# Performance work log

Measured on AMD Instinct MI355X. Metric: run time of the kernel, lower is better.

The kernel has to match this reference:

```python
import jax, jax.numpy as jnp
import numpy as np
from jax import lax

PERIODS = [1, 2, 4, 8]
N = 128  # output_dim // len(periods)
INPUT_DIM = 512
OUTPUT_DIM = 512
BATCH = 64
SEQ = 512


def setup_inputs() -> dict:
    key = jax.random.key(0)
    ks = jax.random.split(key, 32)
    inp = {}
    inp['x'] = jax.random.normal(ks[0], (BATCH, SEQ, INPUT_DIM), dtype=jnp.float32)
    s = 0.05
    inp['W'] = jax.random.normal(ks[1], (INPUT_DIM, OUTPUT_DIM), dtype=jnp.float32) * s
    inp['b'] = jnp.zeros((OUTPUT_DIM,), dtype=jnp.float32)
    inp['Wr'] = jax.random.normal(ks[2], (INPUT_DIM, OUTPUT_DIM), dtype=jnp.float32) * s
    inp['br'] = jnp.zeros((OUTPUT_DIM,), dtype=jnp.float32)
    inp['Wz'] = jax.random.normal(ks[3], (INPUT_DIM, OUTPUT_DIM), dtype=jnp.float32) * s
    inp['bz'] = jnp.zeros((OUTPUT_DIM,), dtype=jnp.float32)
    kidx = 4
    for i in range(len(PERIODS)):
        m = (i + 1) * N
        inp[f'clock_h_{i}'] = jax.random.normal(ks[kidx], (m, N), dtype=jnp.float32) * (1.0 / np.sqrt(m)); kidx += 1
        inp[f'clock_r_{i}'] = jax.random.normal(ks[kidx], (m, m), dtype=jnp.float32) * (1.0 / np.sqrt(m)); kidx += 1
        inp[f'clock_z_{i}'] = jax.random.normal(ks[kidx], (m, N), dtype=jnp.float32) * (1.0 / np.sqrt(m)); kidx += 1
    return inp


def _forward(x, W, b, Wr, br, Wz, bz, clock_h, clock_r, clock_z):
    # x: [B, S, D_in] -> time-major [S, B, D_in]
    Xt = jnp.transpose(x, (1, 0, 2))
    xt = Xt @ W + b      # [S, B, D]
    xrt = Xt @ Wr + br   # [S, B, D]
    xzt = Xt @ Wz + bz   # [S, B, D]
    B = x.shape[0]
    D = W.shape[1]

    def step(h, inputs):
        t, x_t, x_rt, x_zt = inputs
        blocks = []
        for i, period in enumerate(PERIODS):
            m = (i + 1) * N
            hp = h[:, :m]                 # [B, (i+1)n]
            nah = h[:, i * N:(i + 1) * N] # [B, n]
            r = jax.nn.sigmoid(x_rt[:, :m] + hp @ clock_r[i])
            z = jax.nn.sigmoid(x_zt[:, i * N:(i + 1) * N] + hp @ clock_z[i])
            h_new = jax.nn.sigmoid(x_t[:, i * N:(i + 1) * N] + (r * hp) @ clock_h[i])
            v = z * h_new + (1.0 - z) * nah
            blocks.append(jnp.where(t % period == 0, v, nah))
        h_t = jnp.concatenate(blocks, axis=1)
        return h_t, h_t

    times = jnp.arange(x.shape[1])
    h0 = jnp.zeros((B, D), dtype=x.dtype)
    _, hs = lax.scan(step, h0, (times, xt, xrt, xzt))
    # return_sequences=True: back to batch-major [B, S, D]
    return jnp.transpose(hs, (1, 0, 2))


def reference(x, W, b, Wr, br, Wz, bz,
              clock_h_0, clock_r_0, clock_z_0,
              clock_h_1, clock_r_1, clock_z_1,
              clock_h_2, clock_r_2, clock_z_2,
              clock_h_3, clock_r_3, clock_z_3):
    clock_h = [clock_h_0, clock_h_1, clock_h_2, clock_h_3]
    clock_r = [clock_r_0, clock_r_1, clock_r_2, clock_r_3]
    clock_z = [clock_z_0, clock_z_1, clock_z_2, clock_z_3]
    return _forward(x, W, b, Wr, br, Wz, bz, clock_h, clock_r, clock_z)
```

## Files before the change

### kernel.cpp

```cpp
#include <hip/hip_runtime.h>

#define SEQ   512
#define BATCH 64
#define DIM   512

typedef float  f32x4 __attribute__((ext_vector_type(4)));
typedef short  s16x8 __attribute__((ext_vector_type(8)));
typedef __bf16 bf16x2 __attribute__((ext_vector_type(2)));

__device__ __forceinline__ float bits2f(unsigned u) {
  union { unsigned u; float f; } v; v.u = u; return v.f;
}
__device__ __forceinline__ float bf2f(unsigned short h) { return bits2f((unsigned)h << 16); }
__device__ __forceinline__ float bflo(unsigned u) { return bits2f(u << 16); }
__device__ __forceinline__ float bfhi(unsigned u) { return bits2f(u & 0xFFFF0000u); }
__device__ __forceinline__ unsigned short f2bf(float f) {
  union { float f; unsigned u; } v; v.f = f;
  unsigned r = v.u + 0x7FFFu + ((v.u >> 16) & 1u);
  return (unsigned short)(r >> 16);
}
__device__ __forceinline__ unsigned packbf(float lo, float hi) {
  return (unsigned)f2bf(lo) | ((unsigned)f2bf(hi) << 16);
}
__device__ __forceinline__ float sigm(float x) { return 1.0f / (1.0f + __expf(-x)); }

__device__ __forceinline__ float dot2(unsigned w, unsigned h, float acc) {
#if __has_builtin(__builtin_amdgcn_fdot2_f32_bf16)
  return __builtin_amdgcn_fdot2_f32_bf16(__builtin_bit_cast(bf16x2, w),
                                         __builtin_bit_cast(bf16x2, h), acc, false);
#else
  return acc + bflo(w) * bflo(h) + bfhi(w) * bfhi(h);
#endif
}

__device__ __forceinline__ void bar_lds() {
  asm volatile("s_waitcnt lgkmcnt(0)" ::: "memory");
  __builtin_amdgcn_s_barrier();
  asm volatile("" ::: "memory");
}

#define NJOBS 18
struct CastJobs {
  const float* src[NJOBS];
  const float* src2[NJOBS];
  void*        dst[NJOBS];
  int          n[NJOBS];
  int          mode[NJOBS];
  int          m[NJOBS];
  int          iN[NJOBS];
};

__global__ __launch_bounds__(256) void cast_kernel(CastJobs jobs) {
  int gsz = gridDim.x * blockDim.x;
  int gid = blockIdx.x * blockDim.x + threadIdx.x;
  for (int j = 0; j < NJOBS; ++j) {
    int n = jobs.n[j], mode = jobs.mode[j];
    int m = jobs.m[j], iN = jobs.iN[j];
    const float* s = jobs.src[j];
    if (mode == 1) {
      unsigned short* d = (unsigned short*)jobs.dst[j];
      for (int i = gid; i < n; i += gsz) {
        int k = i >> 9, nn = i & 511;
        d[nn * 512 + k] = f2bf(s[i]);
      }
    } else if (mode == 3) {
      unsigned* d = (unsigned*)jobs.dst[j];
      for (int i = gid; i < n; i += gsz) {
        int k2 = i / m, jj = i - k2 * m;
        d[i] = packbf(s[(iN + 2 * k2) * m + jj], s[(iN + 2 * k2 + 1) * m + jj]);
      }
    } else if (mode == 4) {
      unsigned* d = (unsigned*)jobs.dst[j];
      for (int i = gid; i < n; i += gsz) {
        int k2 = i >> 7, jj = i & 127;
        d[i] = packbf(s[(2 * k2) * 128 + jj], s[(2 * k2 + 1) * 128 + jj]);
      }
    } else if (mode == 5) {
      unsigned* d = (unsigned*)jobs.dst[j];
      for (int i = gid; i < n; i += gsz) {
        int k2 = i >> 7, jj = i & 127;
        d[i] = packbf(s[(iN + 2 * k2) * 128 + jj], s[(iN + 2 * k2 + 1) * 128 + jj]);
      }
    } else if (mode == 6) {
      const float* s2 = jobs.src2[j];
      unsigned short* d = (unsigned short*)jobs.dst[j];
      for (int i = gid; i < n; i += gsz) {
        int nrow = i / iN, k = i - nrow * iN;
        float v = (nrow < m) ? s[k * m + nrow] : s2[k * 128 + (nrow - m)];
        d[i] = f2bf(v);
      }
    }
  }
}

__global__ __launch_bounds__(256) void proj_kernel(
    const float* __restrict__ x,
    const unsigned short* __restrict__ WbT,
    const float* __restrict__ bias0, const float* __restrict__ bias1,
    const float* __restrict__ bias2,
    unsigned short* __restrict__ p0, unsigned short* __restrict__ p1,
    unsigned short* __restrict__ p2)
{
  __shared__ __align__(16) unsigned short aS[64 * 40];
  __shared__ __align__(16) unsigned short bS[128 * 40];

  int bx = blockIdx.x;
  int nt = bx % 12, t = bx / 12;
  int wsel = nt >> 2, ncol0 = (nt & 3) * 128;
  const float* bias = (wsel == 0) ? bias0 : (wsel == 1 ? bias1 : bias2);
  unsigned short* pout = (wsel == 0) ? p0 : (wsel == 1 ? p1 : p2);

  int tid = threadIdx.x;
  int wv = tid >> 6, lane = tid & 63;
  int lq = lane & 15, quad = lane >> 4;

  f32x4 acc[8];
#pragma unroll
  for (int s = 0; s < 8; ++s) acc[s] = (f32x4){0.f, 0.f, 0.f, 0.f};

  int arow = tid >> 2, ak0 = (tid & 3) * 8;
  const float* asrc0 = x + ((size_t)arow * SEQ + t) * DIM + ak0;
  int brow = tid >> 1, bk0 = (tid & 1) * 16;
  const unsigned short* bsrc0 =
      WbT + ((size_t)(wsel * 512 + ncol0 + brow)) * 512 + bk0;

  for (int kk = 0; kk < 16; ++kk) {
    const float* asrc = asrc0 + kk * 32;
    float4 f0 = *(const float4*)(asrc);
    float4 f1 = *(const float4*)(asrc + 4);
    uint4 av;
    av.x = packbf(f0.x, f0.y);
    av.y = packbf(f0.z, f0.w);
    av.z = packbf(f1.x, f1.y);
    av.w = packbf(f1.z, f1.w);
    *(uint4*)(aS + arow * 40 + ak0) = av;
    const unsigned short* bsrc = bsrc0 + kk * 32;
    *(uint4*)(bS + brow * 40 + bk0)     = *(const uint4*)(bsrc);
    *(uint4*)(bS + brow * 40 + bk0 + 8) = *(const uint4*)(bsrc + 8);
    __syncthreads();

    s16x8 af = *(const s16x8*)(aS + (wv * 16 + lq) * 40 + quad * 8);
#pragma unroll
    for (int s = 0; s < 8; ++s) {
      s16x8 bf = *(const s16x8*)(bS + (s * 16 + lq) * 40 + quad * 8);
      acc[s] = __builtin_amdgcn_mfma_f32_16x16x32_bf16(af, bf, acc[s], 0, 0, 0);
    }
    __syncthreads();
  }

#pragma unroll
  for (int s = 0; s < 8; ++s) {
    int col = ncol0 + s * 16 + lq;
    float bv = bias[col];
#pragma unroll
    for (int v = 0; v < 4; ++v) {
      int b = wv * 16 + quad * 4 + v;
      pout[((size_t)(t * BATCH + b)) * DIM + col] = f2bf(acc[s][v] + bv);
    }
  }
}

template<int I>
__global__ __launch_bounds__(256) void base_gemm(
    const float* __restrict__ outp,
    const unsigned short* __restrict__ Bcat,
    unsigned short* __restrict__ baseO)
{
  constexpr int KI  = 4 * I;
  constexpr int K   = 128 * I;
  constexpr int NT  = I + 2;
  constexpr int NW  = NT * 128;
  constexpr int PER = 1 << I;

  __shared__ __align__(16) unsigned short aS[64 * 40];
  __shared__ __align__(16) unsigned short bS[128 * 40];

  int bx = blockIdx.x;
  int nt = bx % NT, n = bx / NT;
  int ncol0 = nt * 128;

  int tid = threadIdx.x;
  int wv = tid >> 6, lane = tid & 63;
  int lq = lane & 15, quad = lane >> 4;

  f32x4 acc[8];
#pragma unroll
  for (int s = 0; s < 8; ++s) acc[s] = (f32x4){0.f, 0.f, 0.f, 0.f};

  int arow = tid >> 2, ak0 = (tid & 3) * 8;
  const float* asrc0 = outp + ((size_t)arow * SEQ + (n * PER - 1)) * DIM + ak0;
  int brow = tid >> 1, bk0 = (tid & 1) * 16;
  const unsigned short* bsrc0 = Bcat + (size_t)(ncol0 + brow) * K + bk0;

  for (int kk = 0; kk < KI; ++kk) {
    uint4 av;
    if (n > 0) {
      const float* asrc = asrc0 + kk * 32;
      float4 f0 = *(const float4*)(asrc);
      float4 f1 = *(const float4*)(asrc + 4);
      av.x = packbf(f0.x, f0.y);
      av.y = packbf(f0.z, f0.w);
      av.z = packbf(f1.x, f1.y);
      av.w = packbf(f1.z, f1.w);
    } else {
      av = (uint4){0u, 0u, 0u, 0u};
    }
    *(uint4*)(aS + arow * 40 + ak0) = av;
    const unsigned short* bsrc = bsrc0 + kk * 32;
    *(uint4*)(bS + brow * 40 + bk0)     = *(const uint4*)(bsrc);
    *(uint4*)(bS + brow * 40 + bk0 + 8) = *(const uint4*)(bsrc + 8);
    __syncthreads();

    s16x8 af = *(const s16x8*)(aS + (wv * 16 + lq) * 40 + quad * 8);
#pragma unroll
    for (int s = 0; s < 8; ++s) {
      s16x8 bf = *(const s16x8*)(bS + (s * 16 + lq) * 40 + quad * 8);
      acc[s] = __builtin_amdgcn_mfma_f32_16x16x32_bf16(af, bf, acc[s], 0, 0, 0);
    }
    __syncthreads();
  }

#pragma unroll
  for (int s = 0; s < 8; ++s) {
    int col = ncol0 + s * 16 + lq;
#pragma unroll
    for (int v = 0; v < 4; ++v) {
      int bb = wv * 16 + quad * 4 + v;
      baseO[(size_t)(n * 64 + bb) * NW + col] = f2bf(acc[s][v]);
    }
  }
}

template<int I, int TPB>
__global__ __launch_bounds__(TPB, 1) void scan_phase(
    const unsigned short* __restrict__ px,
    const unsigned short* __restrict__ pr,
    const unsigned short* __restrict__ pz,
    const unsigned* __restrict__ crpk,
    const unsigned* __restrict__ czpk,
    const unsigned* __restrict__ chpk,
    const unsigned short* __restrict__ base,
    float* __restrict__ out)
{
  constexpr int M   = (I + 1) * 128;
  constexpr int IN  = I * 128;
  constexpr int PER = 1 << I;
  constexpr int U   = 512 >> I;
  constexpr int NW  = M + 128;
  constexpr int HKP = M / 2;
  constexpr int SPL = (I == 0) ? 2 : 4;
  constexpr int HT  = HKP / SPL;
  constexpr int ZT  = 64 / SPL;
  constexpr int RTH = (M < TPB) ? M : TPB;

  __shared__ __align__(16) float    hS[128];
  __shared__ __align__(16) unsigned hPk[64];
  __shared__ __align__(16) unsigned uPk[HKP];

  const int b  = blockIdx.x;
  const int t  = threadIdx.x;
  const int jh = t / SPL;
  const int q  = t % SPL;
  const bool hasR = (t < RTH);
  const int col0 = t;

  unsigned wr0[64];
  if (hasR) {
#pragma unroll
    for (int k2 = 0; k2 < 64; ++k2) wr0[k2] = crpk[k2 * M + col0];
  }
  unsigned wz[ZT];
#pragma unroll
  for (int k2 = 0; k2 < ZT; ++k2) wz[k2] = czpk[(q * ZT + k2) * 128 + jh];
  unsigned wh[HT];
#pragma unroll
  for (int k2 = 0; k2 < HT; ++k2) wh[k2] = chpk[(q * HT + k2) * 128 + jh];

  if (t < 128) hS[t] = 0.f;
  if (t < 64)  hPk[t] = 0u;
  float vprev = 0.f;

  unsigned short f_pr = 0, f_pz = 0, f_px = 0, f_br = 0, f_bz = 0;
  float f_pv = 0.f;
  {
    f_pz = (pz + (size_t)b * DIM)[IN + jh];
    f_px = (px + (size_t)b * DIM)[IN + jh];
    if (hasR) f_pr = (pr + (size_t)b * DIM)[col0];
    if constexpr (I > 0) {
      const unsigned short* baseR = base + (size_t)b * NW;
      if (hasR) f_br = baseR[col0];
      f_bz = baseR[M + jh];
    }
  }

  bar_lds();

  for (int n = 0; n < U; ++n) {
    const int s = n * PER;
    const unsigned short c_pr = f_pr, c_pz = f_pz, c_px = f_px;
    const unsigned short c_br = f_br, c_bz = f_bz;
    const float c_pv = f_pv;

    {
      const int n2 = (n + 1 < U) ? (n + 1) : n;
      const int s2 = n2 * PER;
      f_pz = (pz + ((size_t)(s2 * BATCH + b)) * DIM)[IN + jh];
      f_px = (px + ((size_t)(s2 * BATCH + b)) * DIM)[IN + jh];
      if (hasR) f_pr = (pr + ((size_t)(s2 * BATCH + b)) * DIM)[col0];
      if constexpr (I > 0) {
        const unsigned short* baseR = base + (size_t)(n2 * 64 + b) * NW;
        if (hasR) f_br = baseR[col0];
        f_bz = baseR[M + jh];
        if (hasR && col0 < IN)
          f_pv = (out + ((size_t)b * SEQ + (s2 - 1)) * DIM)[col0];
      }
    }

    float az0 = 0.f, az1 = 0.f;
#pragma unroll
    for (int k2 = 0; k2 < ZT; k2 += 2) {
      az0 = dot2(wz[k2],     hPk[q * ZT + k2],     az0);
      az1 = dot2(wz[k2 + 1], hPk[q * ZT + k2 + 1], az1);
    }
    float az = az0 + az1;
    az += __shfl_xor(az, 1);
    if constexpr (SPL == 4) az += __shfl_xor(az, 2);
    float zpre = bf2f(c_pz) + az;
    if constexpr (I > 0) zpre += bf2f(c_bz);
    const float zg = sigm(zpre);

    float u = 0.f;
    if (hasR) {
      float a0 = 0.f, a1 = 0.f, a2 = 0.f, a3 = 0.f;
#pragma unroll
      for (int k2 = 0; k2 < 64; k2 += 4) {
        a0 = dot2(wr0[k2],     hPk[k2],     a0);
        a1 = dot2(wr0[k2 + 1], hPk[k2 + 1], a1);
        a2 = dot2(wr0[k2 + 2], hPk[k2 + 2], a2);
        a3 = dot2(wr0[k2 + 3], hPk[k2 + 3], a3);
      }
      float ar = bf2f(c_pr) + (a0 + a1) + (a2 + a3);
      if constexpr (I > 0) ar += bf2f(c_br);
      const float r = sigm(ar);
      float hp;
      if constexpr (I == 0) hp = hS[col0];
      else hp = (col0 >= IN) ? hS[col0 - IN] : c_pv;
      u = r * hp;
    }
    const float uo = __shfl_xor(u, 1);
    if (hasR && !(t & 1)) uPk[t >> 1] = packbf(u, uo);

    bar_lds();

    float ah0 = 0.f, ah1 = 0.f, ah2 = 0.f, ah3 = 0.f;
    {
      const int o = q * HT;
#pragma unroll
      for (int k2 = 0; k2 < HT; k2 += 4) {
        ah0 = dot2(wh[k2],     uPk[o + k2],     ah0);
        ah1 = dot2(wh[k2 + 1], uPk[o + k2 + 1], ah1);
        ah2 = dot2(wh[k2 + 2], uPk[o + k2 + 2], ah2);
        ah3 = dot2(wh[k2 + 3], uPk[o + k2 + 3], ah3);
      }
    }
    float ah = (ah0 + ah1) + (ah2 + ah3);
    ah += __shfl_xor(ah, 1);
    if constexpr (SPL == 4) ah += __shfl_xor(ah, 2);
    const float hnew = sigm(ah + bf2f(c_px));
    const float v = zg * hnew + (1.f - zg) * vprev;
    vprev = v;

    if (q == 0) hS[jh] = v;
    const float vp = __shfl_xor(v, SPL);
    if ((t & (2 * SPL - 1)) == 0) hPk[t / (2 * SPL)] = packbf(v, vp);

    float* orow = out + ((size_t)b * SEQ + s) * DIM + IN + jh;
#pragma unroll
    for (int p = q; p < PER; p += SPL) orow[p * DIM] = v;

    bar_lds();
  }
}

extern "C" void kernel_launch(void* const* d_in, const int* in_sizes, int n_in,
                              void* d_out, int out_size, void* d_ws, size_t ws_size,
                              hipStream_t stream) {
  (void)in_sizes; (void)n_in; (void)out_size; (void)ws_size;

  const float* x  = (const float*)d_in[0];
  const float* W  = (const float*)d_in[1];
  const float* bb = (const float*)d_in[2];
  const float* Wr = (const float*)d_in[3];
  const float* br = (const float*)d_in[4];
  const float* Wz = (const float*)d_in[5];
  const float* bz = (const float*)d_in[6];
  const float* ch_[4]; const float* cr_[4]; const float* cz_[4];
  for (int i = 0; i < 4; ++i) {
    ch_[i] = (const float*)d_in[7 + 3 * i];
    cr_[i] = (const float*)d_in[8 + 3 * i];
    cz_[i] = (const float*)d_in[9 + 3 * i];
  }

  char* ws = (char*)d_ws;
  size_t off = 0;
  auto alloc = [&](size_t bytes) -> void* {
    void* p = ws + off;
    off += (bytes + 255) & ~(size_t)255;
    return p;
  };

  unsigned short* WbT = (unsigned short*)alloc(3ull * 512 * 512 * 2);
  unsigned* Crpk[4]; unsigned* Chpk[4]; unsigned* Czpk[4];
  unsigned short* Bcat[4] = {nullptr, nullptr, nullptr, nullptr};
  for (int i = 0; i < 4; ++i) {
    int m = (i + 1) * 128;
    Crpk[i] = (unsigned*)alloc((size_t)64 * m * 4);
    Chpk[i] = (unsigned*)alloc((size_t)(m / 2) * 128 * 4);
    Czpk[i] = (unsigned*)alloc((size_t)64 * 128 * 4);
  }
  for (int i = 1; i < 4; ++i) {
    int m = (i + 1) * 128, iN = i * 128;
    Bcat[i] = (unsigned short*)alloc((size_t)(m + 128) * iN * 2);
  }
  unsigned short* p0 = (unsigned short*)alloc((size_t)SEQ * BATCH * DIM * 2);
  unsigned short* p1 = (unsigned short*)alloc((size_t)SEQ * BATCH * DIM * 2);
  unsigned short* p2 = (unsigned short*)alloc((size_t)SEQ * BATCH * DIM * 2);
  unsigned short* baseB = (unsigned short*)alloc((size_t)16384 * 384 * 2);

  CastJobs jobs{};
  int jn = 0;
  const float* wsrc[3] = {W, Wr, Wz};
  for (int j = 0; j < 3; ++j) {
    jobs.src[jn] = wsrc[j]; jobs.dst[jn] = WbT + (size_t)j * 512 * 512;
    jobs.n[jn] = 512 * 512; jobs.mode[jn] = 1; jobs.m[jn] = 512; jobs.iN[jn] = 0; jn++;
  }
  for (int i = 0; i < 4; ++i) {
    int m = (i + 1) * 128, iN = i * 128;
    jobs.src[jn] = cr_[i]; jobs.dst[jn] = Crpk[i];
    jobs.n[jn] = 64 * m; jobs.mode[jn] = 3; jobs.m[jn] = m; jobs.iN[jn] = iN; jn++;
    jobs.src[jn] = ch_[i]; jobs.dst[jn] = Chpk[i];
    jobs.n[jn] = (m / 2) * 128; jobs.mode[jn] = 4; jobs.m[jn] = m; jobs.iN[jn] = iN; jn++;
    jobs.src[jn] = cz_[i]; jobs.dst[jn] = Czpk[i];
    jobs.n[jn] = 64 * 128; jobs.mode[jn] = 5; jobs.m[jn] = m; jobs.iN[jn] = iN; jn++;
  }
  for (int i = 1; i < 4; ++i) {
    int m = (i + 1) * 128, iN = i * 128;
    jobs.src[jn] = cr_[i]; jobs.src2[jn] = cz_[i]; jobs.dst[jn] = Bcat[i];
    jobs.n[jn] = (m + 128) * iN; jobs.mode[jn] = 6; jobs.m[jn] = m; jobs.iN[jn] = iN; jn++;
  }
  cast_kernel<<<256, 256, 0, stream>>>(jobs);

  proj_kernel<<<SEQ * 12, 256, 0, stream>>>(x, WbT, bb, br, bz, p0, p1, p2);

  float* outp = (float*)d_out;

  scan_phase<0, 256><<<64, 256, 0, stream>>>(p0, p1, p2, Crpk[0], Czpk[0],
                                             Chpk[0], nullptr, outp);
  base_gemm<1><<<256 * 3, 256, 0, stream>>>(outp, Bcat[1], baseB);
  scan_phase<1, 512><<<64, 512, 0, stream>>>(p0, p1, p2, Crpk[1], Czpk[1],
                                             Chpk[1], baseB, outp);
  base_gemm<2><<<128 * 4, 256, 0, stream>>>(outp, Bcat[2], baseB);
  scan_phase<2, 512><<<64, 512, 0, stream>>>(p0, p1, p2, Crpk[2], Czpk[2],
                                             Chpk[2], baseB, outp);
  base_gemm<3><<<64 * 5, 256, 0, stream>>>(outp, Bcat[3], baseB);
  scan_phase<3, 512><<<64, 512, 0, stream>>>(p0, p1, p2, Crpk[3], Czpk[3],
                                             Chpk[3], baseB, outp);
}
```

Measured before the change: 1.514 ms.

## Replace phase-0 scan with LDS-resident weights and warp-specialized r/z/h roles

```diff
diff --git a/kernel.cpp b/kernel.cpp
--- a/kernel.cpp
+++ b/kernel.cpp
@@ -33,13 +33,17 @@
 #endif
 }
 
+__device__ __forceinline__ unsigned bcast(unsigned v, int k2) {
+  return (unsigned)__builtin_amdgcn_readlane((int)v, k2);
+}
+
 __device__ __forceinline__ void bar_lds() {
   asm volatile("s_waitcnt lgkmcnt(0)" ::: "memory");
   __builtin_amdgcn_s_barrier();
   asm volatile("" ::: "memory");
 }
 
-#define NJOBS 18
+#define NJOBS 21
 struct CastJobs {
   const float* src[NJOBS];
   const float* src2[NJOBS];
@@ -88,6 +92,12 @@
         int nrow = i / iN, k = i - nrow * iN;
         float v = (nrow < m) ? s[k * m + nrow] : s2[k * 128 + (nrow - m)];
         d[i] = f2bf(v);
+      }
+    } else if (mode == 7) {
+      unsigned* d = (unsigned*)jobs.dst[j];
+      for (int i = gid; i < n; i += gsz) {
+        int c = i >> 6, k2 = i & 63;
+        d[i] = packbf(s[(2 * k2) * 128 + c], s[(2 * k2 + 1) * 128 + c]);
       }
     }
   }
@@ -228,6 +238,117 @@
       int bb = wv * 16 + quad * 4 + v;
       baseO[(size_t)(n * 64 + bb) * NW + col] = f2bf(acc[s][v]);
     }
+  }
+}
+
+#define SCAN0_LDS_BYTES 67072
+
+__global__ __launch_bounds__(384, 1) void scan0_lds(
+    const unsigned short* __restrict__ px,
+    const unsigned short* __restrict__ pr,
+    const unsigned short* __restrict__ pz,
+    const unsigned* __restrict__ CrT,
+    const unsigned* __restrict__ CzT,
+    const unsigned* __restrict__ ChT,
+    float* __restrict__ out)
+{
+  extern __shared__ __align__(16) unsigned char dynLDS[];
+  unsigned* wLDS = (unsigned*)dynLDS;
+  float*    hF   = (float*)(dynLDS + 65536);
+  unsigned* hX   = (unsigned*)(dynLDS + 66048);
+  unsigned* uX   = (unsigned*)(dynLDS + 66304);
+  float*    zX   = (float*)(dynLDS + 66560);
+
+  const int b    = blockIdx.x;
+  const int t    = threadIdx.x;
+  const int lane = t & 63;
+  const bool isR = (t < 128);
+  const bool isH = (t >= 256);
+  const int  jz  = t - 128;
+  const int  jj  = t - 256;
+
+  for (int idx = t; idx < 2 * 128 * 16; idx += 384) {
+    int a = idx >> 11;
+    int rem = idx & 2047;
+    int c = rem >> 4, kq = rem & 15;
+    const unsigned* src = (a == 0) ? CrT : ChT;
+    uint4 v = *(const uint4*)(src + c * 64 + kq * 4);
+    *(uint4*)(wLDS + a * 8192 + c * 64 + (((kq ^ (c & 7)) << 2))) = v;
+  }
+  if (t < 128) hF[t] = 0.f;
+  if (t < 64)  hX[t] = 0u;
+
+  unsigned short f_p;
+  const unsigned short* pp;
+  if (isR)       { f_p = pr[(size_t)b * DIM + t];  pp = pr + ((size_t)BATCH + b) * DIM + t;  }
+  else if (!isH) { f_p = pz[(size_t)b * DIM + jz]; pp = pz + ((size_t)BATCH + b) * DIM + jz; }
+  else           { f_p = px[(size_t)b * DIM + jj]; pp = px + ((size_t)BATCH + b) * DIM + jj; }
+
+  float vprev = 0.f;
+
+  bar_lds();
+
+#pragma unroll 1
+  for (int s = 0; s < SEQ; ++s) {
+    const unsigned short c_p = f_p;
+    if (s + 1 < SEQ) { f_p = *pp; pp += (size_t)BATCH * DIM; }
+
+    if (!isH) {
+      const unsigned hpk = hX[lane];
+      float a0 = 0.f, a1 = 0.f, a2 = 0.f, a3 = 0.f;
+      if (isR) {
+        const unsigned* wb = wLDS + t * 64;
+        const int sw = (t & 7) << 2;
+#pragma unroll
+        for (int kq = 0; kq < 16; ++kq) {
+          uint4 wv = *(const uint4*)(wb + ((kq << 2) ^ sw));
+          a0 = dot2(wv.x, bcast(hpk, 4 * kq + 0), a0);
+          a1 = dot2(wv.y, bcast(hpk, 4 * kq + 1), a1);
+          a2 = dot2(wv.z, bcast(hpk, 4 * kq + 2), a2);
+          a3 = dot2(wv.w, bcast(hpk, 4 * kq + 3), a3);
+        }
+        const float r = sigm(bf2f(c_p) + (a0 + a1) + (a2 + a3));
+        const float u = r * hF[t];
+        const float uo = __shfl_xor(u, 1);
+        if (!(t & 1)) uX[t >> 1] = packbf(u, uo);
+      } else {
+        const uint4* czp = (const uint4*)(CzT + jz * 64);
+#pragma unroll
+        for (int kq = 0; kq < 16; ++kq) {
+          uint4 wv = czp[kq];
+          a0 = dot2(wv.x, bcast(hpk, 4 * kq + 0), a0);
+          a1 = dot2(wv.y, bcast(hpk, 4 * kq + 1), a1);
+          a2 = dot2(wv.z, bcast(hpk, 4 * kq + 2), a2);
+          a3 = dot2(wv.w, bcast(hpk, 4 * kq + 3), a3);
+        }
+        zX[jz] = sigm(bf2f(c_p) + (a0 + a1) + (a2 + a3));
+      }
+    }
+    bar_lds();
+
+    if (isH) {
+      const unsigned upk = uX[lane];
+      const float zf = zX[jj];
+      const unsigned* wb = wLDS + 8192 + jj * 64;
+      const int sw = (jj & 7) << 2;
+      float a0 = 0.f, a1 = 0.f, a2 = 0.f, a3 = 0.f;
+#pragma unroll
+      for (int kq = 0; kq < 16; ++kq) {
+        uint4 wv = *(const uint4*)(wb + ((kq << 2) ^ sw));
+        a0 = dot2(wv.x, bcast(upk, 4 * kq + 0), a0);
+        a1 = dot2(wv.y, bcast(upk, 4 * kq + 1), a1);
+        a2 = dot2(wv.z, bcast(upk, 4 * kq + 2), a2);
+        a3 = dot2(wv.w, bcast(upk, 4 * kq + 3), a3);
+      }
+      const float hnew = sigm(bf2f(c_p) + (a0 + a1) + (a2 + a3));
+      const float v = zf * hnew + (1.f - zf) * vprev;
+      vprev = v;
+      hF[jj] = v;
+      const float vo = __shfl_xor(v, 1);
+      if (!(jj & 1)) hX[jj >> 1] = packbf(v, vo);
+      out[((size_t)b * SEQ + s) * DIM + jj] = v;
+    }
+    bar_lds();
   }
 }
 
@@ -253,9 +374,9 @@
   constexpr int ZT  = 64 / SPL;
   constexpr int RTH = (M < TPB) ? M : TPB;
 
-  __shared__ __align__(16) float    hS[128];
-  __shared__ __align__(16) unsigned hPk[64];
-  __shared__ __align__(16) unsigned uPk[HKP];
+  __shared__ float    hS[128];
+  __shared__ unsigned hPk[64];
+  __shared__ unsigned uPk[HKP];
 
   const int b  = blockIdx.x;
   const int t  = threadIdx.x;
@@ -344,7 +465,7 @@
       const float r = sigm(ar);
       float hp;
       if constexpr (I == 0) hp = hS[col0];
-      else hp = (col0 >= IN) ? hS[col0 - IN] : c_pv;
+      else hp = (col0 >= IN) ? hS[col0 - IN] : (n > 0 ? c_pv : 0.f);
       u = r * hp;
     }
     const float uo = __shfl_xor(u, 1);
@@ -422,6 +543,9 @@
     int m = (i + 1) * 128, iN = i * 128;
     Bcat[i] = (unsigned short*)alloc((size_t)(m + 128) * iN * 2);
   }
+  unsigned* CrT0 = (unsigned*)alloc((size_t)128 * 64 * 4);
+  unsigned* CzT0 = (unsigned*)alloc((size_t)128 * 64 * 4);
+  unsigned* ChT0 = (unsigned*)alloc((size_t)128 * 64 * 4);
   unsigned short* p0 = (unsigned short*)alloc((size_t)SEQ * BATCH * DIM * 2);
   unsigned short* p1 = (unsigned short*)alloc((size_t)SEQ * BATCH * DIM * 2);
   unsigned short* p2 = (unsigned short*)alloc((size_t)SEQ * BATCH * DIM * 2);
@@ -448,14 +572,32 @@
     jobs.src[jn] = cr_[i]; jobs.src2[jn] = cz_[i]; jobs.dst[jn] = Bcat[i];
     jobs.n[jn] = (m + 128) * iN; jobs.mode[jn] = 6; jobs.m[jn] = m; jobs.iN[jn] = iN; jn++;
   }
+  jobs.src[jn] = cr_[0]; jobs.dst[jn] = CrT0;
+  jobs.n[jn] = 128 * 64; jobs.mode[jn] = 7; jobs.m[jn] = 128; jobs.iN[jn] = 0; jn++;
+  jobs.src[jn] = cz_[0]; jobs.dst[jn] = CzT0;
+  jobs.n[jn] = 128 * 64; jobs.mode[jn] = 7; jobs.m[jn] = 128; jobs.iN[jn] = 0; jn++;
+  jobs.src[jn] = ch_[0]; jobs.dst[jn] = ChT0;
+  jobs.n[jn] = 128 * 64; jobs.mode[jn] = 7; jobs.m[jn] = 128; jobs.iN[jn] = 0; jn++;
   cast_kernel<<<256, 256, 0, stream>>>(jobs);
 
   proj_kernel<<<SEQ * 12, 256, 0, stream>>>(x, WbT, bb, br, bz, p0, p1, p2);
 
   float* outp = (float*)d_out;
 
-  scan_phase<0, 256><<<64, 256, 0, stream>>>(p0, p1, p2, Crpk[0], Czpk[0],
-                                             Chpk[0], nullptr, outp);
+  static bool s_attr = false;
+  if (!s_attr) {
+    (void)hipFuncSetAttribute((const void*)scan0_lds,
+                              hipFuncAttributeMaxDynamicSharedMemorySize,
+                              SCAN0_LDS_BYTES);
+    s_attr = true;
+  }
+  (void)hipGetLastError();
+  scan0_lds<<<64, 384, SCAN0_LDS_BYTES, stream>>>(p0, p1, p2, CrT0, CzT0, ChT0,
+                                                  outp);
+  if (hipGetLastError() != hipSuccess) {
+    scan_phase<0, 256><<<64, 256, 0, stream>>>(p0, p1, p2, Crpk[0], Czpk[0],
+                                               Chpk[0], nullptr, outp);
+  }
   base_gemm<1><<<256 * 3, 256, 0, stream>>>(outp, Bcat[1], baseB);
   scan_phase<1, 512><<<64, 512, 0, stream>>>(p0, p1, p2, Crpk[1], Czpk[1],
                                              Chpk[1], baseB, outp);
```

Result: slower. 2.499 ms (+65.1%).
